# Kernel optimization log

Hardware: AMD Instinct MI355X
Metric: run time of the kernel (lower is better)

Reference implementation:

```python
import jax, jax.numpy as jnp
import numpy as np

NORM = 1.0  # normalization_factor


def _glorot(key, shape):
    fan_in, fan_out = shape
    lim = float(np.sqrt(6.0 / (fan_in + fan_out)))
    return jax.random.uniform(key, shape, jnp.float32, -lim, lim)


def setup_inputs() -> dict:
    key = jax.random.key(0)
    ks = jax.random.split(key, 12)
    B, N = 8, 2048
    latent, hidden, out_dim = 64, 128, 64
    inp = {
        "latent_features": jax.random.normal(ks[0], (B, N, latent), jnp.float32),
        "adjacency_matrix": jax.random.uniform(ks[1], (B, N, N), jnp.float32),
        "node_mask": jnp.ones((B, N, 1), jnp.float32),
        # 3 GCN layers: latent->hidden, hidden->hidden, hidden->hidden
        "W0": _glorot(ks[2], (latent, hidden)), "b0": jnp.zeros((hidden,), jnp.float32),
        "W1": _glorot(ks[3], (hidden, hidden)), "b1": jnp.zeros((hidden,), jnp.float32),
        "W2": _glorot(ks[4], (hidden, hidden)), "b2": jnp.zeros((hidden,), jnp.float32),
        # output projection hidden->out_dim
        "Wout": _glorot(ks[5], (hidden, out_dim)), "bout": jnp.zeros((out_dim,), jnp.float32),
    }
    return inp


def _gcn_layer(h, adj, W, b):
    # message transform (linear), gather+sum aggregate via dense adjacency, ReLU act
    msg = h @ W + b                      # [B,N,dout]
    agg = jnp.einsum('bij,bjd->bid', adj, msg) / NORM  # sum aggregation over neighbors
    return jax.nn.relu(agg)


def reference(latent_features, adjacency_matrix, node_mask,
              W0, b0, W1, b1, W2, b2, Wout, bout):
    h = _gcn_layer(latent_features, adjacency_matrix, W0, b0)
    h = _gcn_layer(h, adjacency_matrix, W1, b1)
    h = _gcn_layer(h, adjacency_matrix, W2, b2)
    # output projection + node mask
    return (h @ Wout + bout) * node_mask
```

## Files before the change

### kernel.cpp

```cpp
#include <hip/hip_runtime.h>
#include <hip/hip_bf16.h>


typedef __bf16 bf16;
typedef __bf16 bf16x4 __attribute__((ext_vector_type(4)));
typedef __bf16 bf16x8 __attribute__((ext_vector_type(8)));
typedef float  f32x16 __attribute__((ext_vector_type(16)));
typedef float  f32x4  __attribute__((ext_vector_type(4)));

static __device__ inline f32x16 mfma32(bf16x8 a, bf16x8 b, f32x16 c) {
    return __builtin_amdgcn_mfma_f32_32x32x16_bf16(a, b, c, 0, 0, 0);
}

static __device__ inline void tile_barrier() {
    asm volatile("s_waitcnt lgkmcnt(0)" ::: "memory");
    __builtin_amdgcn_s_barrier();
    asm volatile("" ::: "memory");
}

#define NB   8
#define NN   2048
#define LAT  64
#define HID  128
#define ODIM 64
#define BM   64
#define BK   128
#define NP   16
#define LDK  136

__global__ __launch_bounds__(256) void prep_t0_k(
    const float* __restrict__ lat, const float* __restrict__ W0,
    const float* __restrict__ b0,
    const float* __restrict__ W1, const float* __restrict__ W2,
    const float* __restrict__ Wout,
    bf16* __restrict__ msgT, bf16* __restrict__ WT1,
    bf16* __restrict__ WT2, bf16* __restrict__ WoutT)
{
    __shared__ __align__(16) bf16 WTs[HID * 72];
    int tid = threadIdx.x;
    int blk = blockIdx.x;

    if (blk >= 256) {
        int i = (blk - 256) * 256 + tid;
        if (i < HID * HID) { int fo = i >> 7, k = i & 127; WT1[i] = (bf16)W1[k * HID + fo]; return; }
        i -= HID * HID;
        if (i < HID * HID) { int fo = i >> 7, k = i & 127; WT2[i] = (bf16)W2[k * HID + fo]; return; }
        i -= HID * HID;
        if (i < ODIM * HID) { int o = i >> 7, k = i & 127; WoutT[i] = (bf16)Wout[k * ODIM + o]; return; }
        return;
    }

    for (int i = tid; i < LAT * HID; i += 256) {
        int k = i >> 7, fo = i & 127;
        WTs[fo * 72 + k] = (bf16)W0[i];
    }
    __syncthreads();

    int l = tid & 63, w = tid >> 6;
    int lm = l & 31, lh = l >> 5;
    int g0 = blk * 64;
    int b  = g0 >> 11, nb = g0 & 2047;

    const bf16*  Wrow = &WTs[(w * 32 + lm) * 72 + lh * 8];
    const float* r0   = lat + (size_t)(g0 + lm) * LAT + lh * 8;
    const float* r1   = r0 + (size_t)32 * LAT;

    f32x16 acc0 = {}, acc1 = {};
#pragma unroll
    for (int k0 = 0; k0 < LAT; k0 += 16) {
        bf16x8 a = *(const bf16x8*)(Wrow + k0);
        f32x4 x0 = *(const f32x4*)(r0 + k0), x1 = *(const f32x4*)(r0 + k0 + 4);
        f32x4 y0 = *(const f32x4*)(r1 + k0), y1 = *(const f32x4*)(r1 + k0 + 4);
        bf16x8 v0, v1;
        v0[0]=(bf16)x0[0]; v0[1]=(bf16)x0[1]; v0[2]=(bf16)x0[2]; v0[3]=(bf16)x0[3];
        v0[4]=(bf16)x1[0]; v0[5]=(bf16)x1[1]; v0[6]=(bf16)x1[2]; v0[7]=(bf16)x1[3];
        v1[0]=(bf16)y0[0]; v1[1]=(bf16)y0[1]; v1[2]=(bf16)y0[2]; v1[3]=(bf16)y0[3];
        v1[4]=(bf16)y1[0]; v1[5]=(bf16)y1[1]; v1[6]=(bf16)y1[2]; v1[7]=(bf16)y1[3];
        acc0 = mfma32(a, v0, acc0);
        acc1 = mfma32(a, v1, acc1);
    }

    bf16* outb = msgT + (size_t)b * (HID * NN) + nb;
#pragma unroll
    for (int r = 0; r < 16; ++r) {
        int fo = w * 32 + (r & 3) + 8 * (r >> 2) + 4 * lh;
        float bv = b0[fo];
        outb[(size_t)fo * NN + lm]      = (bf16)(acc0[r] + bv);
        outb[(size_t)fo * NN + 32 + lm] = (bf16)(acc1[r] + bv);
    }
}

template<int MODE, int ADJW>
__global__ __launch_bounds__(512) void agg_k(
    const float* __restrict__ adjf, const bf16* __restrict__ adjbi,
    bf16* __restrict__ adjbo,
    const bf16* __restrict__ msgT, const bf16* __restrict__ WTn,
    const float* __restrict__ biasn, bf16* __restrict__ msg_out,
    const float* __restrict__ mask, float* __restrict__ out)
{
    __shared__ __align__(16) bf16 As[2][BM * LDK];
    __shared__ __align__(16) bf16 Bs[2][HID * LDK];
    __shared__ __align__(16) bf16 Hs[BM * LDK];
    int tid = threadIdx.x;
    int l = tid & 63, w = tid >> 6;
    int lm = l & 31, lh = l >> 5;
    int wm = w >> 2, wn = w & 3;
    int b  = blockIdx.x & 7;
    int m0 = (blockIdx.x >> 3) * BM;

    const bf16* msgb = msgT + (size_t)b * (HID * NN);
    int br = tid >> 3, bc8 = (tid & 7) * 8;
    const bf16* bsrc = msgb + (size_t)br * NN + bc8;

    int ar = tid >> 3, acf = (tid & 7) * 4;
    const float* asrc = (ADJW == 0) ? adjf + (size_t)b * NN * NN + (size_t)(m0 + ar) * NN + acf : nullptr;
    bf16* adst = (ADJW == 0) ? adjbo + (size_t)b * NN * NN + (size_t)(m0 + ar) * NN + acf : nullptr;
    int ac8 = (tid & 7) * 8;
    const bf16* asrcb = (ADJW == 1) ? adjbi + (size_t)b * NN * NN + (size_t)(m0 + ar) * NN + ac8 : nullptr;

    f32x4  fa[2][4];
    bf16x8 ba[2][2];
    bf16x8 pb[2][4];

    auto loadTile = [&](int set, int k) {
        if (ADJW == 0) {
#pragma unroll
            for (int g = 0; g < 4; ++g) fa[set][g] = *(const f32x4*)(asrc + k + g * 32);
        } else {
#pragma unroll
            for (int g = 0; g < 2; ++g) ba[set][g] = *(const bf16x8*)(asrcb + k + g * 64);
        }
#pragma unroll
        for (int h = 0; h < 2; ++h)
#pragma unroll
            for (int g = 0; g < 2; ++g)
                pb[set][h * 2 + g] = *(const bf16x8*)(bsrc + (size_t)(h * 64) * NN + k + g * 64);
    };
    auto storeTile = [&](int set, int buf, int k) {
        if (ADJW == 0) {
#pragma unroll
            for (int g = 0; g < 4; ++g) {
                bf16x4 v;
                v[0]=(bf16)fa[set][g][0]; v[1]=(bf16)fa[set][g][1];
                v[2]=(bf16)fa[set][g][2]; v[3]=(bf16)fa[set][g][3];
                *(bf16x4*)&As[buf][ar * LDK + acf + g * 32] = v;
                *(bf16x4*)(adst + k + g * 32)               = v;
            }
        } else {
#pragma unroll
            for (int g = 0; g < 2; ++g)
                *(bf16x8*)&As[buf][ar * LDK + ac8 + g * 64] = ba[set][g];
        }
#pragma unroll
        for (int h = 0; h < 2; ++h)
#pragma unroll
            for (int g = 0; g < 2; ++g)
                *(bf16x8*)&Bs[buf][(br + h * 64) * LDK + bc8 + g * 64] = pb[set][h * 2 + g];
    };

    f32x16 acc = {};
    auto mfmaTile = [&](int buf) {
        const bf16* Ac = &As[buf][(wm * 32 + lm) * LDK + lh * 8];
        const bf16* Bc = &Bs[buf][(wn * 32 + lm) * LDK + lh * 8];
#pragma unroll
        for (int s = 0; s < 8; ++s)
            acc = mfma32(*(const bf16x8*)(Ac + s * 16), *(const bf16x8*)(Bc + s * 16), acc);
    };

    loadTile(0, 0 * BK);
    loadTile(1, 1 * BK);
    storeTile(0, 0, 0 * BK);
    tile_barrier();

#define PHASE(U)                                                               \
    do {                                                                       \
        int q = qb + (U);                                                      \
        if (q + 2 < NP) loadTile((U), (q + 2) * BK);                           \
        if (q + 1 < NP) storeTile(((U) + 1) & 1, ((U) + 1) & 1, (q + 1) * BK); \
        mfmaTile((U) & 1);                                                     \
        tile_barrier();                                                        \
    } while (0)

#pragma unroll 1
    for (int qb = 0; qb < NP; qb += 2) {
        PHASE(0);
        PHASE(1);
    }
#undef PHASE

#pragma unroll
    for (int r = 0; r < 16; ++r) {
        int row = wm * 32 + (r & 3) + 8 * (r >> 2) + 4 * lh;
        float v = acc[r];
        Hs[row * LDK + wn * 32 + lm] = (bf16)(v > 0.f ? v : 0.f);
    }
    __syncthreads();

    if (MODE == 0) {
        const bf16* Arow = WTn + (size_t)(wn * 32 + lm) * HID + lh * 8;
        const bf16* Brow = &Hs[(wm * 32 + lm) * LDK + lh * 8];
        f32x16 acc2 = {};
#pragma unroll
        for (int s = 0; s < 8; ++s)
            acc2 = mfma32(*(const bf16x8*)(Arow + s * 16), *(const bf16x8*)(Brow + s * 16), acc2);
        bf16* outb = msg_out + (size_t)b * (HID * NN) + m0 + wm * 32;
#pragma unroll
        for (int r = 0; r < 16; ++r) {
            int fo = wn * 32 + (r & 3) + 8 * (r >> 2) + 4 * lh;
            outb[(size_t)fo * NN + lm] = (bf16)(acc2[r] + biasn[fo]);
        }
    } else {
        if (wn < 2) {
            int ob = wn * 32;
            const bf16* Arow = &Hs[(wm * 32 + lm) * LDK + lh * 8];
            const bf16* Brow = WTn + (size_t)(ob + lm) * HID + lh * 8;
            f32x16 acc2 = {};
#pragma unroll
            for (int s = 0; s < 8; ++s)
                acc2 = mfma32(*(const bf16x8*)(Arow + s * 16), *(const bf16x8*)(Brow + s * 16), acc2);
            float bv = biasn[ob + lm];
#pragma unroll
            for (int r = 0; r < 16; ++r) {
                int node = wm * 32 + (r & 3) + 8 * (r >> 2) + 4 * lh;
                int g = b * NN + m0 + node;
                out[(size_t)g * ODIM + ob + lm] = (acc2[r] + bv) * mask[g];
            }
        }
    }
}

extern "C" void kernel_launch(void* const* d_in, const int* in_sizes, int n_in,
                              void* d_out, int out_size, void* d_ws, size_t ws_size,
                              hipStream_t stream)
{
    const float* lat  = (const float*)d_in[0];
    const float* adj  = (const float*)d_in[1];
    const float* mask = (const float*)d_in[2];
    const float* W0   = (const float*)d_in[3];
    const float* b0   = (const float*)d_in[4];
    const float* W1   = (const float*)d_in[5];
    const float* b1   = (const float*)d_in[6];
    const float* W2   = (const float*)d_in[7];
    const float* b2   = (const float*)d_in[8];
    const float* Wout = (const float*)d_in[9];
    const float* bout = (const float*)d_in[10];
    float* out = (float*)d_out;

    char* ws = (char*)d_ws;
    bf16* msgA  = (bf16*)(ws + 0);
    bf16* msgB  = (bf16*)(ws + 4194304);
    bf16* adjbf = (bf16*)(ws + 8388608);
    bf16* WT1   = (bf16*)(ws + 75497472);
    bf16* WT2   = (bf16*)(ws + 75530240);
    bf16* WoutT = (bf16*)(ws + 75563008);

    prep_t0_k<<<416, 256, 0, stream>>>(lat, W0, b0, W1, W2, Wout, msgA, WT1, WT2, WoutT);

    agg_k<0, 0><<<256, 512, 0, stream>>>(adj, nullptr, adjbf, msgA, WT1, b1, msgB, nullptr, nullptr);
    agg_k<0, 1><<<256, 512, 0, stream>>>(nullptr, adjbf, nullptr, msgB, WT2, b2, msgA, nullptr, nullptr);
    agg_k<1, 1><<<256, 512, 0, stream>>>(nullptr, adjbf, nullptr, msgA, WoutT, bout, nullptr, mask, out);
}
```

Measured before the change: 267.8 us.

## Stage tiles via direct global-to-LDS loads with XOR swizzle; hoist adj conversion

Moves the fp32-to-bf16 adjacency conversion out of the first aggregation kernel into extra blocks of the prep kernel, so all three aggregation launches share one bf16 path. Operand tiles are now staged with global_load_lds straight into unpadded, XOR-swizzled LDS buffers instead of passing through registers. The loop waits with vmcnt counters and two barriers per step. This is meant to cut register pressure and VALU work during staging and to avoid LDS bank conflicts without padding. It risks more barrier stalls and leaves the conversion pass serialized ahead of the first aggregation.

```diff
diff --git a/kernel.cpp b/kernel.cpp
--- a/kernel.cpp
+++ b/kernel.cpp
@@ -3,7 +3,6 @@
 
 
 typedef __bf16 bf16;
-typedef __bf16 bf16x4 __attribute__((ext_vector_type(4)));
 typedef __bf16 bf16x8 __attribute__((ext_vector_type(8)));
 typedef float  f32x16 __attribute__((ext_vector_type(16)));
 typedef float  f32x4  __attribute__((ext_vector_type(4)));
@@ -12,10 +11,10 @@
     return __builtin_amdgcn_mfma_f32_32x32x16_bf16(a, b, c, 0, 0, 0);
 }
 
-static __device__ inline void tile_barrier() {
-    asm volatile("s_waitcnt lgkmcnt(0)" ::: "memory");
-    __builtin_amdgcn_s_barrier();
-    asm volatile("" ::: "memory");
+static __device__ inline void glds16(const bf16* g, bf16* l) {
+    __builtin_amdgcn_global_load_lds(
+        (const __attribute__((address_space(1))) unsigned int*)g,
+        (__attribute__((address_space(3))) unsigned int*)l, 16, 0, 0);
 }
 
 #define NB   8
@@ -26,19 +25,36 @@
 #define BM   64
 #define BK   128
 #define NP   16
-#define LDK  136
+#define HLD  136
 
 __global__ __launch_bounds__(256) void prep_t0_k(
-    const float* __restrict__ lat, const float* __restrict__ W0,
-    const float* __restrict__ b0,
+    const float* __restrict__ lat, const float* __restrict__ adj,
+    const float* __restrict__ W0, const float* __restrict__ b0,
     const float* __restrict__ W1, const float* __restrict__ W2,
     const float* __restrict__ Wout,
-    bf16* __restrict__ msgT, bf16* __restrict__ WT1,
-    bf16* __restrict__ WT2, bf16* __restrict__ WoutT)
+    bf16* __restrict__ msgT, bf16* __restrict__ adjb,
+    bf16* __restrict__ WT1, bf16* __restrict__ WT2, bf16* __restrict__ WoutT)
 {
     __shared__ __align__(16) bf16 WTs[HID * 72];
     int tid = threadIdx.x;
     int blk = blockIdx.x;
+
+    if (blk >= 416) {
+        size_t base = (size_t)(blk - 416) * 16384;
+        const float* s = adj + base;
+        bf16* d = adjb + base;
+#pragma unroll
+        for (int j = 0; j < 8; ++j) {
+            int off = j * 2048 + tid * 8;
+            f32x4 x0 = *(const f32x4*)(s + off);
+            f32x4 x1 = *(const f32x4*)(s + off + 4);
+            bf16x8 v;
+            v[0]=(bf16)x0[0]; v[1]=(bf16)x0[1]; v[2]=(bf16)x0[2]; v[3]=(bf16)x0[3];
+            v[4]=(bf16)x1[0]; v[5]=(bf16)x1[1]; v[6]=(bf16)x1[2]; v[7]=(bf16)x1[3];
+            *(bf16x8*)(d + off) = v;
+        }
+        return;
+    }
 
     if (blk >= 256) {
         int i = (blk - 256) * 256 + tid;
@@ -90,115 +106,85 @@
     }
 }
 
-template<int MODE, int ADJW>
+template<int MODE>
 __global__ __launch_bounds__(512) void agg_k(
-    const float* __restrict__ adjf, const bf16* __restrict__ adjbi,
-    bf16* __restrict__ adjbo,
+    const bf16* __restrict__ adjb,
     const bf16* __restrict__ msgT, const bf16* __restrict__ WTn,
     const float* __restrict__ biasn, bf16* __restrict__ msg_out,
     const float* __restrict__ mask, float* __restrict__ out)
 {
-    __shared__ __align__(16) bf16 As[2][BM * LDK];
-    __shared__ __align__(16) bf16 Bs[2][HID * LDK];
-    __shared__ __align__(16) bf16 Hs[BM * LDK];
+    __shared__ __align__(16) bf16 As[2][BM * BK];
+    __shared__ __align__(16) bf16 Bs[2][HID * BK];
+    __shared__ __align__(16) bf16 Hs[BM * HLD];
     int tid = threadIdx.x;
-    int l = tid & 63, w = tid >> 6;
+    int l = tid & 63, wv = tid >> 6;
     int lm = l & 31, lh = l >> 5;
-    int wm = w >> 2, wn = w & 3;
+    int wm = wv >> 2, wn = wv & 3;
     int b  = blockIdx.x & 7;
     int m0 = (blockIdx.x >> 3) * BM;
 
-    const bf16* msgb = msgT + (size_t)b * (HID * NN);
-    int br = tid >> 3, bc8 = (tid & 7) * 8;
-    const bf16* bsrc = msgb + (size_t)br * NN + bc8;
-
-    int ar = tid >> 3, acf = (tid & 7) * 4;
-    const float* asrc = (ADJW == 0) ? adjf + (size_t)b * NN * NN + (size_t)(m0 + ar) * NN + acf : nullptr;
-    bf16* adst = (ADJW == 0) ? adjbo + (size_t)b * NN * NN + (size_t)(m0 + ar) * NN + acf : nullptr;
-    int ac8 = (tid & 7) * 8;
-    const bf16* asrcb = (ADJW == 1) ? adjbi + (size_t)b * NN * NN + (size_t)(m0 + ar) * NN + ac8 : nullptr;
-
-    f32x4  fa[2][4];
-    bf16x8 ba[2][2];
-    bf16x8 pb[2][4];
-
-    auto loadTile = [&](int set, int k) {
-        if (ADJW == 0) {
-#pragma unroll
-            for (int g = 0; g < 4; ++g) fa[set][g] = *(const f32x4*)(asrc + k + g * 32);
-        } else {
-#pragma unroll
-            for (int g = 0; g < 2; ++g) ba[set][g] = *(const bf16x8*)(asrcb + k + g * 64);
-        }
-#pragma unroll
-        for (int h = 0; h < 2; ++h)
-#pragma unroll
-            for (int g = 0; g < 2; ++g)
-                pb[set][h * 2 + g] = *(const bf16x8*)(bsrc + (size_t)(h * 64) * NN + k + g * 64);
-    };
-    auto storeTile = [&](int set, int buf, int k) {
-        if (ADJW == 0) {
-#pragma unroll
-            for (int g = 0; g < 4; ++g) {
-                bf16x4 v;
-                v[0]=(bf16)fa[set][g][0]; v[1]=(bf16)fa[set][g][1];
-                v[2]=(bf16)fa[set][g][2]; v[3]=(bf16)fa[set][g][3];
-                *(bf16x4*)&As[buf][ar * LDK + acf + g * 32] = v;
-                *(bf16x4*)(adst + k + g * 32)               = v;
-            }
-        } else {
-#pragma unroll
-            for (int g = 0; g < 2; ++g)
-                *(bf16x8*)&As[buf][ar * LDK + ac8 + g * 64] = ba[set][g];
-        }
-#pragma unroll
-        for (int h = 0; h < 2; ++h)
-#pragma unroll
-            for (int g = 0; g < 2; ++g)
-                *(bf16x8*)&Bs[buf][(br + h * 64) * LDK + bc8 + g * 64] = pb[set][h * 2 + g];
+    int r4 = l >> 4, c16 = l & 15;
+
+    const bf16* adjbase = adjb + (size_t)b * NN * NN + (size_t)m0 * NN;
+    const bf16* msgb    = msgT + (size_t)b * (HID * NN);
+
+    int ar0 = wv * 8 + r4, ar1 = ar0 + 4;
+    const bf16* aS0 = adjbase + (size_t)ar0 * NN + ((c16 ^ (ar0 & 7)) * 8);
+    const bf16* aS1 = adjbase + (size_t)ar1 * NN + ((c16 ^ (ar1 & 7)) * 8);
+    int br0 = wv * 16 + r4;
+    const bf16* bS0 = msgb + (size_t)(br0     ) * NN + ((c16 ^ ((br0     ) & 7)) * 8);
+    const bf16* bS1 = msgb + (size_t)(br0 +  4) * NN + ((c16 ^ ((br0 +  4) & 7)) * 8);
+    const bf16* bS2 = msgb + (size_t)(br0 +  8) * NN + ((c16 ^ ((br0 +  8) & 7)) * 8);
+    const bf16* bS3 = msgb + (size_t)(br0 + 12) * NN + ((c16 ^ ((br0 + 12) & 7)) * 8);
+
+    auto stage = [&](int buf, int k) {
+        glds16(aS0 + k, &As[buf][(wv * 8     ) * BK]);
+        glds16(aS1 + k, &As[buf][(wv * 8 +  4) * BK]);
+        glds16(bS0 + k, &Bs[buf][(wv * 16    ) * BK]);
+        glds16(bS1 + k, &Bs[buf][(wv * 16 + 4) * BK]);
+        glds16(bS2 + k, &Bs[buf][(wv * 16 + 8) * BK]);
+        glds16(bS3 + k, &Bs[buf][(wv * 16 +12) * BK]);
     };
 
     f32x16 acc = {};
     auto mfmaTile = [&](int buf) {
-        const bf16* Ac = &As[buf][(wm * 32 + lm) * LDK + lh * 8];
-        const bf16* Bc = &Bs[buf][(wn * 32 + lm) * LDK + lh * 8];
-#pragma unroll
-        for (int s = 0; s < 8; ++s)
-            acc = mfma32(*(const bf16x8*)(Ac + s * 16), *(const bf16x8*)(Bc + s * 16), acc);
+        int arow = wm * 32 + lm;
+        int brow = wn * 32 + lm;
+        const bf16* Abase = &As[buf][arow * BK];
+        const bf16* Bbase = &Bs[buf][brow * BK];
+        int h = lm & 7;
+#pragma unroll
+        for (int s = 0; s < 8; ++s) {
+            int ca = ((lh + 2 * s) ^ h) * 8;
+            acc = mfma32(*(const bf16x8*)(Abase + ca), *(const bf16x8*)(Bbase + ca), acc);
+        }
     };
 
-    loadTile(0, 0 * BK);
-    loadTile(1, 1 * BK);
-    storeTile(0, 0, 0 * BK);
-    tile_barrier();
-
-#define PHASE(U)                                                               \
-    do {                                                                       \
-        int q = qb + (U);                                                      \
-        if (q + 2 < NP) loadTile((U), (q + 2) * BK);                           \
-        if (q + 1 < NP) storeTile(((U) + 1) & 1, ((U) + 1) & 1, (q + 1) * BK); \
-        mfmaTile((U) & 1);                                                     \
-        tile_barrier();                                                        \
-    } while (0)
+    stage(0, 0);
+    stage(1, BK);
 
 #pragma unroll 1
-    for (int qb = 0; qb < NP; qb += 2) {
-        PHASE(0);
-        PHASE(1);
-    }
-#undef PHASE
+    for (int t = 0; t < NP; ++t) {
+        if (t < NP - 1) asm volatile("s_waitcnt vmcnt(6)" ::: "memory");
+        else            asm volatile("s_waitcnt vmcnt(0)" ::: "memory");
+        __builtin_amdgcn_s_barrier();
+        mfmaTile(t & 1);
+        asm volatile("" ::: "memory");
+        __builtin_amdgcn_s_barrier();
+        if (t + 2 < NP) stage(t & 1, (t + 2) * BK);
+    }
 
 #pragma unroll
     for (int r = 0; r < 16; ++r) {
         int row = wm * 32 + (r & 3) + 8 * (r >> 2) + 4 * lh;
         float v = acc[r];
-        Hs[row * LDK + wn * 32 + lm] = (bf16)(v > 0.f ? v : 0.f);
+        Hs[row * HLD + wn * 32 + lm] = (bf16)(v > 0.f ? v : 0.f);
     }
     __syncthreads();
 
     if (MODE == 0) {
         const bf16* Arow = WTn + (size_t)(wn * 32 + lm) * HID + lh * 8;
-        const bf16* Brow = &Hs[(wm * 32 + lm) * LDK + lh * 8];
+        const bf16* Brow = &Hs[(wm * 32 + lm) * HLD + lh * 8];
         f32x16 acc2 = {};
 #pragma unroll
         for (int s = 0; s < 8; ++s)
@@ -212,7 +198,7 @@
     } else {
         if (wn < 2) {
             int ob = wn * 32;
-            const bf16* Arow = &Hs[(wm * 32 + lm) * LDK + lh * 8];
+            const bf16* Arow = &Hs[(wm * 32 + lm) * HLD + lh * 8];
             const bf16* Brow = WTn + (size_t)(ob + lm) * HID + lh * 8;
             f32x16 acc2 = {};
 #pragma unroll
@@ -254,9 +240,10 @@
     bf16* WT2   = (bf16*)(ws + 75530240);
     bf16* WoutT = (bf16*)(ws + 75563008);
 
-    prep_t0_k<<<416, 256, 0, stream>>>(lat, W0, b0, W1, W2, Wout, msgA, WT1, WT2, WoutT);
-
-    agg_k<0, 0><<<256, 512, 0, stream>>>(adj, nullptr, adjbf, msgA, WT1, b1, msgB, nullptr, nullptr);
-    agg_k<0, 1><<<256, 512, 0, stream>>>(nullptr, adjbf, nullptr, msgB, WT2, b2, msgA, nullptr, nullptr);
-    agg_k<1, 1><<<256, 512, 0, stream>>>(nullptr, adjbf, nullptr, msgA, WoutT, bout, nullptr, mask, out);
-}
+    prep_t0_k<<<2464, 256, 0, stream>>>(lat, adj, W0, b0, W1, W2, Wout,
+                                        msgA, adjbf, WT1, WT2, WoutT);
+
+    agg_k<0><<<256, 512, 0, stream>>>(adjbf, msgA, WT1, b1, msgB, nullptr, nullptr);
+    agg_k<0><<<256, 512, 0, stream>>>(adjbf, msgB, WT2, b2, msgA, nullptr, nullptr);
+    agg_k<1><<<256, 512, 0, stream>>>(adjbf, msgA, WoutT, bout, nullptr, mask, out);
+}
```

Result: slower. 296.9 us (+10.9%).

## Use direct global-to-LDS loads with XOR swizzle for bf16 aggregation layers

Applied to the files above, without the earlier changes.

Splits the aggregation kernel into an fp32-adjacency version for the first layer and a new bf16 version for layers two and three. The new version stages adjacency and message tiles with global_load_lds (direct global-to-LDS DMA), uses an XOR-swizzled unpadded LDS layout to avoid bank conflicts, and drives a double-buffered pipeline with explicit vmcnt waits. The aim is to cut register staging and VGPR pressure in the memory-bound layers. The price is hand-tuned waitcnt accounting, which is easy to get wrong, and only two buffers in flight.

```diff
diff --git a/kernel.cpp b/kernel.cpp
--- a/kernel.cpp
+++ b/kernel.cpp
@@ -16,6 +16,12 @@
     asm volatile("s_waitcnt lgkmcnt(0)" ::: "memory");
     __builtin_amdgcn_s_barrier();
     asm volatile("" ::: "memory");
+}
+
+static __device__ inline void glds16(const bf16* g, bf16* l) {
+    __builtin_amdgcn_global_load_lds(
+        (const __attribute__((address_space(1))) unsigned int*)g,
+        (__attribute__((address_space(3))) unsigned int*)l, 16, 0, 0);
 }
 
 #define NB   8
@@ -27,6 +33,7 @@
 #define BK   128
 #define NP   16
 #define LDK  136
+#define HLD  136
 
 __global__ __launch_bounds__(256) void prep_t0_k(
     const float* __restrict__ lat, const float* __restrict__ W0,
@@ -90,17 +97,14 @@
     }
 }
 
-template<int MODE, int ADJW>
-__global__ __launch_bounds__(512) void agg_k(
-    const float* __restrict__ adjf, const bf16* __restrict__ adjbi,
-    bf16* __restrict__ adjbo,
+__global__ __launch_bounds__(512) void agg_f32_k(
+    const float* __restrict__ adjf, bf16* __restrict__ adjbo,
     const bf16* __restrict__ msgT, const bf16* __restrict__ WTn,
-    const float* __restrict__ biasn, bf16* __restrict__ msg_out,
-    const float* __restrict__ mask, float* __restrict__ out)
+    const float* __restrict__ biasn, bf16* __restrict__ msg_out)
 {
     __shared__ __align__(16) bf16 As[2][BM * LDK];
     __shared__ __align__(16) bf16 Bs[2][HID * LDK];
-    __shared__ __align__(16) bf16 Hs[BM * LDK];
+    __shared__ __align__(16) bf16 Hs[BM * HLD];
     int tid = threadIdx.x;
     int l = tid & 63, w = tid >> 6;
     int lm = l & 31, lh = l >> 5;
@@ -113,23 +117,15 @@
     const bf16* bsrc = msgb + (size_t)br * NN + bc8;
 
     int ar = tid >> 3, acf = (tid & 7) * 4;
-    const float* asrc = (ADJW == 0) ? adjf + (size_t)b * NN * NN + (size_t)(m0 + ar) * NN + acf : nullptr;
-    bf16* adst = (ADJW == 0) ? adjbo + (size_t)b * NN * NN + (size_t)(m0 + ar) * NN + acf : nullptr;
-    int ac8 = (tid & 7) * 8;
-    const bf16* asrcb = (ADJW == 1) ? adjbi + (size_t)b * NN * NN + (size_t)(m0 + ar) * NN + ac8 : nullptr;
+    const float* asrc = adjf  + (size_t)b * NN * NN + (size_t)(m0 + ar) * NN + acf;
+    bf16*        adst = adjbo + (size_t)b * NN * NN + (size_t)(m0 + ar) * NN + acf;
 
     f32x4  fa[2][4];
-    bf16x8 ba[2][2];
     bf16x8 pb[2][4];
 
     auto loadTile = [&](int set, int k) {
-        if (ADJW == 0) {
-#pragma unroll
-            for (int g = 0; g < 4; ++g) fa[set][g] = *(const f32x4*)(asrc + k + g * 32);
-        } else {
-#pragma unroll
-            for (int g = 0; g < 2; ++g) ba[set][g] = *(const bf16x8*)(asrcb + k + g * 64);
-        }
+#pragma unroll
+        for (int g = 0; g < 4; ++g) fa[set][g] = *(const f32x4*)(asrc + k + g * 32);
 #pragma unroll
         for (int h = 0; h < 2; ++h)
 #pragma unroll
@@ -137,19 +133,13 @@
                 pb[set][h * 2 + g] = *(const bf16x8*)(bsrc + (size_t)(h * 64) * NN + k + g * 64);
     };
     auto storeTile = [&](int set, int buf, int k) {
-        if (ADJW == 0) {
-#pragma unroll
-            for (int g = 0; g < 4; ++g) {
-                bf16x4 v;
-                v[0]=(bf16)fa[set][g][0]; v[1]=(bf16)fa[set][g][1];
-                v[2]=(bf16)fa[set][g][2]; v[3]=(bf16)fa[set][g][3];
-                *(bf16x4*)&As[buf][ar * LDK + acf + g * 32] = v;
-                *(bf16x4*)(adst + k + g * 32)               = v;
-            }
-        } else {
-#pragma unroll
-            for (int g = 0; g < 2; ++g)
-                *(bf16x8*)&As[buf][ar * LDK + ac8 + g * 64] = ba[set][g];
+#pragma unroll
+        for (int g = 0; g < 4; ++g) {
+            bf16x4 v;
+            v[0]=(bf16)fa[set][g][0]; v[1]=(bf16)fa[set][g][1];
+            v[2]=(bf16)fa[set][g][2]; v[3]=(bf16)fa[set][g][3];
+            *(bf16x4*)&As[buf][ar * LDK + acf + g * 32] = v;
+            *(bf16x4*)(adst + k + g * 32)               = v;
         }
 #pragma unroll
         for (int h = 0; h < 2; ++h)
@@ -192,13 +182,103 @@
     for (int r = 0; r < 16; ++r) {
         int row = wm * 32 + (r & 3) + 8 * (r >> 2) + 4 * lh;
         float v = acc[r];
-        Hs[row * LDK + wn * 32 + lm] = (bf16)(v > 0.f ? v : 0.f);
+        Hs[row * HLD + wn * 32 + lm] = (bf16)(v > 0.f ? v : 0.f);
+    }
+    __syncthreads();
+
+    const bf16* Arow = WTn + (size_t)(wn * 32 + lm) * HID + lh * 8;
+    const bf16* Brow = &Hs[(wm * 32 + lm) * HLD + lh * 8];
+    f32x16 acc2 = {};
+#pragma unroll
+    for (int s = 0; s < 8; ++s)
+        acc2 = mfma32(*(const bf16x8*)(Arow + s * 16), *(const bf16x8*)(Brow + s * 16), acc2);
+    bf16* outb = msg_out + (size_t)b * (HID * NN) + m0 + wm * 32;
+#pragma unroll
+    for (int r = 0; r < 16; ++r) {
+        int fo = wn * 32 + (r & 3) + 8 * (r >> 2) + 4 * lh;
+        outb[(size_t)fo * NN + lm] = (bf16)(acc2[r] + biasn[fo]);
+    }
+}
+
+template<int MODE>
+__global__ __launch_bounds__(512) void aggg_k(
+    const bf16* __restrict__ adjb,
+    const bf16* __restrict__ msgT, const bf16* __restrict__ WTn,
+    const float* __restrict__ biasn, bf16* __restrict__ msg_out,
+    const float* __restrict__ mask, float* __restrict__ out)
+{
+    __shared__ __align__(16) bf16 As[2][BM * BK];
+    __shared__ __align__(16) bf16 Bs[2][HID * BK];
+    __shared__ __align__(16) bf16 Hs[BM * HLD];
+    int tid = threadIdx.x;
+    int l = tid & 63, wv = tid >> 6;
+    int lm = l & 31, lh = l >> 5;
+    int wm = wv >> 2, wn = wv & 3;
+    int b  = blockIdx.x & 7;
+    int m0 = (blockIdx.x >> 3) * BM;
+
+    int r4 = l >> 4, c16 = l & 15;
+
+    const bf16* adjbase = adjb + (size_t)b * NN * NN + (size_t)m0 * NN;
+    const bf16* msgb    = msgT + (size_t)b * (HID * NN);
+
+    int ar0 = wv * 8 + r4, ar1 = ar0 + 4;
+    const bf16* aS0 = adjbase + (size_t)ar0 * NN + ((c16 ^ (ar0 & 7)) * 8);
+    const bf16* aS1 = adjbase + (size_t)ar1 * NN + ((c16 ^ (ar1 & 7)) * 8);
+    int br0 = wv * 16 + r4;
+    const bf16* bS0 = msgb + (size_t)(br0     ) * NN + ((c16 ^ ((br0     ) & 7)) * 8);
+    const bf16* bS1 = msgb + (size_t)(br0 +  4) * NN + ((c16 ^ ((br0 +  4) & 7)) * 8);
+    const bf16* bS2 = msgb + (size_t)(br0 +  8) * NN + ((c16 ^ ((br0 +  8) & 7)) * 8);
+    const bf16* bS3 = msgb + (size_t)(br0 + 12) * NN + ((c16 ^ ((br0 + 12) & 7)) * 8);
+
+    auto stage = [&](int buf, int k) {
+        glds16(aS0 + k, &As[buf][(wv * 8     ) * BK]);
+        glds16(aS1 + k, &As[buf][(wv * 8 +  4) * BK]);
+        glds16(bS0 + k, &Bs[buf][(wv * 16    ) * BK]);
+        glds16(bS1 + k, &Bs[buf][(wv * 16 + 4) * BK]);
+        glds16(bS2 + k, &Bs[buf][(wv * 16 + 8) * BK]);
+        glds16(bS3 + k, &Bs[buf][(wv * 16 +12) * BK]);
+    };
+
+    f32x16 acc = {};
+    auto mfmaTile = [&](int buf) {
+        int arow = wm * 32 + lm;
+        int brow = wn * 32 + lm;
+        const bf16* Abase = &As[buf][arow * BK];
+        const bf16* Bbase = &Bs[buf][brow * BK];
+        int h = lm & 7;
+#pragma unroll
+        for (int s = 0; s < 8; ++s) {
+            int ca = ((lh + 2 * s) ^ h) * 8;
+            acc = mfma32(*(const bf16x8*)(Abase + ca), *(const bf16x8*)(Bbase + ca), acc);
+        }
+    };
+
+    stage(0, 0);
+    stage(1, BK);
+
+#pragma unroll 1
+    for (int t = 0; t < NP; ++t) {
+        if (t < NP - 1) asm volatile("s_waitcnt vmcnt(6)" ::: "memory");
+        else            asm volatile("s_waitcnt vmcnt(0)" ::: "memory");
+        __builtin_amdgcn_s_barrier();
+        mfmaTile(t & 1);
+        asm volatile("" ::: "memory");
+        __builtin_amdgcn_s_barrier();
+        if (t + 2 < NP) stage(t & 1, (t + 2) * BK);
+    }
+
+#pragma unroll
+    for (int r = 0; r < 16; ++r) {
+        int row = wm * 32 + (r & 3) + 8 * (r >> 2) + 4 * lh;
+        float v = acc[r];
+        Hs[row * HLD + wn * 32 + lm] = (bf16)(v > 0.f ? v : 0.f);
     }
     __syncthreads();
 
     if (MODE == 0) {
         const bf16* Arow = WTn + (size_t)(wn * 32 + lm) * HID + lh * 8;
-        const bf16* Brow = &Hs[(wm * 32 + lm) * LDK + lh * 8];
+        const bf16* Brow = &Hs[(wm * 32 + lm) * HLD + lh * 8];
         f32x16 acc2 = {};
 #pragma unroll
         for (int s = 0; s < 8; ++s)
@@ -212,7 +292,7 @@
     } else {
         if (wn < 2) {
             int ob = wn * 32;
-            const bf16* Arow = &Hs[(wm * 32 + lm) * LDK + lh * 8];
+            const bf16* Arow = &Hs[(wm * 32 + lm) * HLD + lh * 8];
             const bf16* Brow = WTn + (size_t)(ob + lm) * HID + lh * 8;
             f32x16 acc2 = {};
 #pragma unroll
@@ -256,7 +336,7 @@
 
     prep_t0_k<<<416, 256, 0, stream>>>(lat, W0, b0, W1, W2, Wout, msgA, WT1, WT2, WoutT);
 
-    agg_k<0, 0><<<256, 512, 0, stream>>>(adj, nullptr, adjbf, msgA, WT1, b1, msgB, nullptr, nullptr);
-    agg_k<0, 1><<<256, 512, 0, stream>>>(nullptr, adjbf, nullptr, msgB, WT2, b2, msgA, nullptr, nullptr);
-    agg_k<1, 1><<<256, 512, 0, stream>>>(nullptr, adjbf, nullptr, msgA, WoutT, bout, nullptr, mask, out);
-}
+    agg_f32_k<<<256, 512, 0, stream>>>(adj, adjbf, msgA, WT1, b1, msgB);
+    aggg_k<0><<<256, 512, 0, stream>>>(adjbf, msgB, WT2, b2, msgA, nullptr, nullptr);
+    aggg_k<1><<<256, 512, 0, stream>>>(adjbf, msgA, WoutT, bout, nullptr, mask, out);
+}
```

New measurement: 278.7 us. 1.04x slower.

## Split-K the bf16 aggregation layers with separate combine kernel

Applied to the files above, without the earlier changes.

Layers two and three now split the neighbour reduction into two K halves handled by separate blocks, doubling the grid to 512 blocks with smaller LDS tiles and a 4-blocks-per-CU launch bound. Each half writes fp32 partial sums to workspace, and a new combine kernel sums them, applies ReLU and performs the following weight projection. This aims to fill the GPU better and hide memory latency on the adjacency stream. In exchange it adds extra kernel launches and fp32 partial-sum traffic through global memory.

```diff
diff --git a/kernel.cpp b/kernel.cpp
--- a/kernel.cpp
+++ b/kernel.cpp
@@ -27,6 +27,10 @@
 #define BK   128
 #define NP   16
 #define LDK  136
+#define HLD  136
+#define SKK  64
+#define SKP  16
+#define SKL  72
 
 __global__ __launch_bounds__(256) void prep_t0_k(
     const float* __restrict__ lat, const float* __restrict__ W0,
@@ -90,17 +94,14 @@
     }
 }
 
-template<int MODE, int ADJW>
-__global__ __launch_bounds__(512) void agg_k(
-    const float* __restrict__ adjf, const bf16* __restrict__ adjbi,
-    bf16* __restrict__ adjbo,
+__global__ __launch_bounds__(512) void agg_f32_k(
+    const float* __restrict__ adjf, bf16* __restrict__ adjbo,
     const bf16* __restrict__ msgT, const bf16* __restrict__ WTn,
-    const float* __restrict__ biasn, bf16* __restrict__ msg_out,
-    const float* __restrict__ mask, float* __restrict__ out)
+    const float* __restrict__ biasn, bf16* __restrict__ msg_out)
 {
     __shared__ __align__(16) bf16 As[2][BM * LDK];
     __shared__ __align__(16) bf16 Bs[2][HID * LDK];
-    __shared__ __align__(16) bf16 Hs[BM * LDK];
+    __shared__ __align__(16) bf16 Hs[BM * HLD];
     int tid = threadIdx.x;
     int l = tid & 63, w = tid >> 6;
     int lm = l & 31, lh = l >> 5;
@@ -113,23 +114,15 @@
     const bf16* bsrc = msgb + (size_t)br * NN + bc8;
 
     int ar = tid >> 3, acf = (tid & 7) * 4;
-    const float* asrc = (ADJW == 0) ? adjf + (size_t)b * NN * NN + (size_t)(m0 + ar) * NN + acf : nullptr;
-    bf16* adst = (ADJW == 0) ? adjbo + (size_t)b * NN * NN + (size_t)(m0 + ar) * NN + acf : nullptr;
-    int ac8 = (tid & 7) * 8;
-    const bf16* asrcb = (ADJW == 1) ? adjbi + (size_t)b * NN * NN + (size_t)(m0 + ar) * NN + ac8 : nullptr;
+    const float* asrc = adjf  + (size_t)b * NN * NN + (size_t)(m0 + ar) * NN + acf;
+    bf16*        adst = adjbo + (size_t)b * NN * NN + (size_t)(m0 + ar) * NN + acf;
 
     f32x4  fa[2][4];
-    bf16x8 ba[2][2];
     bf16x8 pb[2][4];
 
     auto loadTile = [&](int set, int k) {
-        if (ADJW == 0) {
-#pragma unroll
-            for (int g = 0; g < 4; ++g) fa[set][g] = *(const f32x4*)(asrc + k + g * 32);
-        } else {
-#pragma unroll
-            for (int g = 0; g < 2; ++g) ba[set][g] = *(const bf16x8*)(asrcb + k + g * 64);
-        }
+#pragma unroll
+        for (int g = 0; g < 4; ++g) fa[set][g] = *(const f32x4*)(asrc + k + g * 32);
 #pragma unroll
         for (int h = 0; h < 2; ++h)
 #pragma unroll
@@ -137,19 +130,13 @@
                 pb[set][h * 2 + g] = *(const bf16x8*)(bsrc + (size_t)(h * 64) * NN + k + g * 64);
     };
     auto storeTile = [&](int set, int buf, int k) {
-        if (ADJW == 0) {
-#pragma unroll
-            for (int g = 0; g < 4; ++g) {
-                bf16x4 v;
-                v[0]=(bf16)fa[set][g][0]; v[1]=(bf16)fa[set][g][1];
-                v[2]=(bf16)fa[set][g][2]; v[3]=(bf16)fa[set][g][3];
-                *(bf16x4*)&As[buf][ar * LDK + acf + g * 32] = v;
-                *(bf16x4*)(adst + k + g * 32)               = v;
-            }
-        } else {
-#pragma unroll
-            for (int g = 0; g < 2; ++g)
-                *(bf16x8*)&As[buf][ar * LDK + ac8 + g * 64] = ba[set][g];
+#pragma unroll
+        for (int g = 0; g < 4; ++g) {
+            bf16x4 v;
+            v[0]=(bf16)fa[set][g][0]; v[1]=(bf16)fa[set][g][1];
+            v[2]=(bf16)fa[set][g][2]; v[3]=(bf16)fa[set][g][3];
+            *(bf16x4*)&As[buf][ar * LDK + acf + g * 32] = v;
+            *(bf16x4*)(adst + k + g * 32)               = v;
         }
 #pragma unroll
         for (int h = 0; h < 2; ++h)
@@ -192,38 +179,159 @@
     for (int r = 0; r < 16; ++r) {
         int row = wm * 32 + (r & 3) + 8 * (r >> 2) + 4 * lh;
         float v = acc[r];
-        Hs[row * LDK + wn * 32 + lm] = (bf16)(v > 0.f ? v : 0.f);
+        Hs[row * HLD + wn * 32 + lm] = (bf16)(v > 0.f ? v : 0.f);
+    }
+    __syncthreads();
+
+    const bf16* Arow = WTn + (size_t)(wn * 32 + lm) * HID + lh * 8;
+    const bf16* Brow = &Hs[(wm * 32 + lm) * HLD + lh * 8];
+    f32x16 acc2 = {};
+#pragma unroll
+    for (int s = 0; s < 8; ++s)
+        acc2 = mfma32(*(const bf16x8*)(Arow + s * 16), *(const bf16x8*)(Brow + s * 16), acc2);
+    bf16* outb = msg_out + (size_t)b * (HID * NN) + m0 + wm * 32;
+#pragma unroll
+    for (int r = 0; r < 16; ++r) {
+        int fo = wn * 32 + (r & 3) + 8 * (r >> 2) + 4 * lh;
+        outb[(size_t)fo * NN + lm] = (bf16)(acc2[r] + biasn[fo]);
+    }
+}
+
+__global__ __launch_bounds__(512, 4) void aggsk_k(
+    const bf16* __restrict__ adjb, const bf16* __restrict__ msgT,
+    float* __restrict__ hpart)
+{
+    __shared__ __align__(16) bf16 As[2][BM * SKL];
+    __shared__ __align__(16) bf16 Bs[2][HID * SKL];
+    int tid = threadIdx.x;
+    int l = tid & 63, w = tid >> 6;
+    int lm = l & 31, lh = l >> 5;
+    int wm = w >> 2, wn = w & 3;
+    int blk = blockIdx.x;
+    int b  = blk & 7;
+    int s  = (blk >> 3) & 1;
+    int m0 = (blk >> 4) * BM;
+    int k0 = s * (NN / 2);
+
+    const bf16* msgb = msgT + (size_t)b * (HID * NN) + k0;
+    int br = tid >> 3, bc8 = (tid & 7) * 8;
+    const bf16* bsrc = msgb + (size_t)br * NN + bc8;
+
+    int ar = tid >> 3, ac8 = (tid & 7) * 8;
+    const bf16* asrc = adjb + (size_t)b * NN * NN + (size_t)(m0 + ar) * NN + k0 + ac8;
+
+    bf16x8 ba[2];
+    bf16x8 pb[2][2];
+
+    auto loadTile = [&](int set, int k) {
+        ba[set] = *(const bf16x8*)(asrc + k);
+        pb[set][0] = *(const bf16x8*)(bsrc + k);
+        pb[set][1] = *(const bf16x8*)(bsrc + (size_t)64 * NN + k);
+    };
+    auto storeTile = [&](int set, int buf) {
+        *(bf16x8*)&As[buf][ar * SKL + ac8]        = ba[set];
+        *(bf16x8*)&Bs[buf][br * SKL + bc8]        = pb[set][0];
+        *(bf16x8*)&Bs[buf][(br + 64) * SKL + bc8] = pb[set][1];
+    };
+
+    f32x16 acc = {};
+    auto mfmaTile = [&](int buf) {
+        const bf16* Ac = &As[buf][(wm * 32 + lm) * SKL + lh * 8];
+        const bf16* Bc = &Bs[buf][(wn * 32 + lm) * SKL + lh * 8];
+#pragma unroll
+        for (int q = 0; q < 4; ++q)
+            acc = mfma32(*(const bf16x8*)(Ac + q * 16), *(const bf16x8*)(Bc + q * 16), acc);
+    };
+
+    loadTile(0, 0 * SKK);
+    loadTile(1, 1 * SKK);
+    storeTile(0, 0);
+    tile_barrier();
+
+#define PHASE(U)                                                   \
+    do {                                                           \
+        int q = qb + (U);                                          \
+        if (q + 2 < SKP) loadTile((U), (q + 2) * SKK);             \
+        if (q + 1 < SKP) storeTile(((U) + 1) & 1, ((U) + 1) & 1);  \
+        mfmaTile((U) & 1);                                         \
+        tile_barrier();                                            \
+    } while (0)
+
+#pragma unroll 1
+    for (int qb = 0; qb < SKP; qb += 2) {
+        PHASE(0);
+        PHASE(1);
+    }
+#undef PHASE
+
+    float* hp = hpart + ((size_t)((b << 1) | s) * NN + m0 + wm * 32) * HID + wn * 32 + lm;
+#pragma unroll
+    for (int r = 0; r < 16; ++r) {
+        int row = (r & 3) + 8 * (r >> 2) + 4 * lh;
+        hp[(size_t)row * HID] = acc[r];
+        hp += 0;
+    }
+}
+
+template<int MODE>
+__global__ __launch_bounds__(512) void comb_k(
+    const float* __restrict__ hpart, const bf16* __restrict__ WTn,
+    const float* __restrict__ biasn, bf16* __restrict__ msg_out,
+    const float* __restrict__ mask, float* __restrict__ out)
+{
+    __shared__ __align__(16) bf16 Hs[BM * HLD];
+    int tid = threadIdx.x;
+    int l = tid & 63, w = tid >> 6;
+    int lm = l & 31, lh = l >> 5;
+    int wm = w >> 2, wn = w & 3;
+    int b  = blockIdx.x & 7;
+    int m0 = (blockIdx.x >> 3) * BM;
+
+    int r = tid >> 3, c = (tid & 7) * 16;
+    const float* p0 = hpart + ((size_t)(b * 2 + 0) * NN + m0 + r) * HID + c;
+    const float* p1 = hpart + ((size_t)(b * 2 + 1) * NN + m0 + r) * HID + c;
+#pragma unroll
+    for (int i = 0; i < 4; ++i) {
+        f32x4 x = *(const f32x4*)(p0 + i * 4);
+        f32x4 y = *(const f32x4*)(p1 + i * 4);
+        bf16x4 v;
+#pragma unroll
+        for (int j = 0; j < 4; ++j) {
+            float z = x[j] + y[j];
+            v[j] = (bf16)(z > 0.f ? z : 0.f);
+        }
+        *(bf16x4*)&Hs[r * HLD + c + i * 4] = v;
     }
     __syncthreads();
 
     if (MODE == 0) {
         const bf16* Arow = WTn + (size_t)(wn * 32 + lm) * HID + lh * 8;
-        const bf16* Brow = &Hs[(wm * 32 + lm) * LDK + lh * 8];
+        const bf16* Brow = &Hs[(wm * 32 + lm) * HLD + lh * 8];
         f32x16 acc2 = {};
 #pragma unroll
-        for (int s = 0; s < 8; ++s)
-            acc2 = mfma32(*(const bf16x8*)(Arow + s * 16), *(const bf16x8*)(Brow + s * 16), acc2);
+        for (int q = 0; q < 8; ++q)
+            acc2 = mfma32(*(const bf16x8*)(Arow + q * 16), *(const bf16x8*)(Brow + q * 16), acc2);
         bf16* outb = msg_out + (size_t)b * (HID * NN) + m0 + wm * 32;
 #pragma unroll
-        for (int r = 0; r < 16; ++r) {
-            int fo = wn * 32 + (r & 3) + 8 * (r >> 2) + 4 * lh;
-            outb[(size_t)fo * NN + lm] = (bf16)(acc2[r] + biasn[fo]);
+        for (int rr = 0; rr < 16; ++rr) {
+            int fo = wn * 32 + (rr & 3) + 8 * (rr >> 2) + 4 * lh;
+            outb[(size_t)fo * NN + lm] = (bf16)(acc2[rr] + biasn[fo]);
         }
     } else {
         if (wn < 2) {
             int ob = wn * 32;
-            const bf16* Arow = &Hs[(wm * 32 + lm) * LDK + lh * 8];
+            const bf16* Arow = &Hs[(wm * 32 + lm) * HLD + lh * 8];
             const bf16* Brow = WTn + (size_t)(ob + lm) * HID + lh * 8;
             f32x16 acc2 = {};
 #pragma unroll
-            for (int s = 0; s < 8; ++s)
-                acc2 = mfma32(*(const bf16x8*)(Arow + s * 16), *(const bf16x8*)(Brow + s * 16), acc2);
+            for (int q = 0; q < 8; ++q)
+                acc2 = mfma32(*(const bf16x8*)(Arow + q * 16), *(const bf16x8*)(Brow + q * 16), acc2);
             float bv = biasn[ob + lm];
 #pragma unroll
-            for (int r = 0; r < 16; ++r) {
-                int node = wm * 32 + (r & 3) + 8 * (r >> 2) + 4 * lh;
+            for (int rr = 0; rr < 16; ++rr) {
+                int node = wm * 32 + (rr & 3) + 8 * (rr >> 2) + 4 * lh;
                 int g = b * NN + m0 + node;
-                out[(size_t)g * ODIM + ob + lm] = (acc2[r] + bv) * mask[g];
+                out[(size_t)g * ODIM + ob + lm] = (acc2[rr] + bv) * mask[g];
             }
         }
     }
@@ -247,16 +355,21 @@
     float* out = (float*)d_out;
 
     char* ws = (char*)d_ws;
-    bf16* msgA  = (bf16*)(ws + 0);
-    bf16* msgB  = (bf16*)(ws + 4194304);
-    bf16* adjbf = (bf16*)(ws + 8388608);
-    bf16* WT1   = (bf16*)(ws + 75497472);
-    bf16* WT2   = (bf16*)(ws + 75530240);
-    bf16* WoutT = (bf16*)(ws + 75563008);
+    bf16*  msgA  = (bf16*)(ws + 0);
+    bf16*  msgB  = (bf16*)(ws + 4194304);
+    bf16*  adjbf = (bf16*)(ws + 8388608);
+    bf16*  WT1   = (bf16*)(ws + 75497472);
+    bf16*  WT2   = (bf16*)(ws + 75530240);
+    bf16*  WoutT = (bf16*)(ws + 75563008);
+    float* hpart = (float*)(ws + 83886080);
 
     prep_t0_k<<<416, 256, 0, stream>>>(lat, W0, b0, W1, W2, Wout, msgA, WT1, WT2, WoutT);
 
-    agg_k<0, 0><<<256, 512, 0, stream>>>(adj, nullptr, adjbf, msgA, WT1, b1, msgB, nullptr, nullptr);
-    agg_k<0, 1><<<256, 512, 0, stream>>>(nullptr, adjbf, nullptr, msgB, WT2, b2, msgA, nullptr, nullptr);
-    agg_k<1, 1><<<256, 512, 0, stream>>>(nullptr, adjbf, nullptr, msgA, WoutT, bout, nullptr, mask, out);
-}
+    agg_f32_k<<<256, 512, 0, stream>>>(adj, adjbf, msgA, WT1, b1, msgB);
+
+    aggsk_k<<<512, 512, 0, stream>>>(adjbf, msgB, hpart);
+    comb_k<0><<<256, 512, 0, stream>>>(hpart, WT2, b2, msgA, nullptr, nullptr);
+
+    aggsk_k<<<512, 512, 0, stream>>>(adjbf, msgA, hpart);
+    comb_k<1><<<256, 512, 0, stream>>>(hpart, WoutT, bout, nullptr, mask, out);
+}
```

Result: slower. 276.4 us (+3.2%).
